# Kernel tuning notes

Hardware: AMD Instinct MI355X
Metric: run time of the kernel (lower is better)

The kernel has to match this reference:

```python
import jax, jax.numpy as jnp
import numpy as np

BN_EPS = 1e-5
LEAKY_SLOPE = 0.2


def setup_inputs() -> dict:
    key = jax.random.key(0)
    kx, kw, kg, kb = jax.random.split(key, 4)
    B, C, N, Cout, k = 8, 64, 4096, 64, 20
    x = jax.random.normal(kx, (B, C, N), dtype=jnp.float32)
    # Conv2d(2C -> Cout, kernel 1x1, bias=False) weight, stored as [Cout, 2C]
    W = jax.random.normal(kw, (Cout, 2 * C), dtype=jnp.float32) * 0.05
    gamma = jnp.ones((Cout,), dtype=jnp.float32) + 0.01 * jax.random.normal(kg, (Cout,), dtype=jnp.float32)
    beta = 0.01 * jax.random.normal(kb, (Cout,), dtype=jnp.float32)
    return {"x": x, "W": W, "gamma": gamma, "beta": beta, "k": k}


def reference(x, W, gamma, beta, k):
    # x: [B, C, N]
    B, C, N = x.shape
    # --- kNN graph on first 3 channels (xyz) ---
    xyz = jnp.transpose(x[:, :3, :], (0, 2, 1))              # [B, N, 3]
    sq = jnp.sum(xyz * xyz, axis=-1)                          # [B, N]
    dist = sq[:, :, None] + sq[:, None, :] - 2.0 * jnp.einsum('bnc,bmc->bnm', xyz, xyz)  # [B, N, N]
    _, idx = jax.lax.top_k(-dist, k + 1)                      # smallest distances, sorted
    edges = idx[:, :, 1:]                                     # drop self -> [B, N, k]

    # --- gather neighbor features ---
    xn = jnp.transpose(x, (0, 2, 1))                          # [B, N, C]
    nbrs = xn[jnp.arange(B)[:, None, None], edges]            # [B, N, k, C]
    central = xn[:, :, None, :]                               # [B, N, 1, C]
    edge_feat = jnp.concatenate(
        [jnp.broadcast_to(central, nbrs.shape), nbrs - central], axis=-1)  # [B, N, k, 2C]

    # --- 1x1 conv (pointwise matmul) ---
    h = jnp.einsum('bnkc,oc->bnko', edge_feat, W)             # [B, N, k, Cout]

    # --- BatchNorm2d (training-mode batch stats over B, k, N per channel) ---
    mean = jnp.mean(h, axis=(0, 1, 2))
    var = jnp.var(h, axis=(0, 1, 2))
    hn = (h - mean) * jax.lax.rsqrt(var + BN_EPS) * gamma + beta

    # --- LeakyReLU(0.2) then max over k neighbors ---
    act = jnp.where(hn >= 0, hn, LEAKY_SLOPE * hn)
    out = jnp.max(act, axis=2)                                # [B, N, Cout]
    return jnp.transpose(out, (0, 2, 1))                      # [B, Cout, N]
```

## Files before the change

kernel.cpp:

```cpp
#include <hip/hip_runtime.h>
#include <math.h>

#define BB 8
#define CC 64
#define NN 4096
#define COUT 64
#define KK 20
#define NQ 32768

__device__ __forceinline__ float np_sq(float ax, float ay, float az) {
    return __fadd_rn(__fadd_rn(__fmul_rn(ax, ax), __fmul_rn(ay, ay)), __fmul_rn(az, az));
}
__device__ __forceinline__ float np_dist(float qx, float qy, float qz, float sqn, float4 p) {
    float dot = __fadd_rn(__fadd_rn(__fmul_rn(qx, p.x), __fmul_rn(qy, p.y)), __fmul_rn(qz, p.z));
    return __fsub_rn(__fadd_rn(sqn, p.w), __fmul_rn(2.0f, dot));
}
__device__ __forceinline__ float min3f(float a, float b, float c) { return fminf(fminf(a, b), c); }
__device__ __forceinline__ float max3f(float a, float b, float c) { return fmaxf(fmaxf(a, b), c); }

__global__ __launch_bounds__(256) void prep_kernel(const float* __restrict__ x,
                                                   float4* __restrict__ pts4) {
    int g = blockIdx.x * 256 + threadIdx.x;
    int b = g >> 12, n = g & (NN - 1);
    const float* xb = x + (size_t)b * CC * NN;
    float ax = xb[n], ay = xb[NN + n], az = xb[2 * NN + n];
    pts4[g] = make_float4(ax, ay, az, np_sq(ax, ay, az));
}

template <int NCH, int SLOTS>
__global__ __launch_bounds__(256) void knn_part(const float4* __restrict__ pts4,
                                                float* __restrict__ pd) {
    constexpr int CH = NN / NCH;
    const int grp = blockIdx.x / NCH;
    const int ch = blockIdx.x % NCH;
    const int tid = threadIdx.x;
    const int q = grp * 256 + tid;
    const int b = q >> 12;
    const int n = q & (NN - 1);
    const float4* pb = pts4 + (size_t)b * NN;

    __shared__ float4 pts[CH];
    for (int i = tid; i < CH; i += 256) pts[i] = pb[ch * CH + i];
    __syncthreads();

    float4 me = pb[n];
    const float qx = me.x, qy = me.y, qz = me.z, sqn = me.w;

    float bd[SLOTS];
#pragma unroll
    for (int i = 0; i < SLOTS; ++i) bd[i] = INFINITY;

#pragma unroll 4
    for (int i = 0; i < CH; i += 4) {
        float4 p0 = pts[i + 0], p1 = pts[i + 1], p2 = pts[i + 2], p3 = pts[i + 3];
        float d0 = np_dist(qx, qy, qz, sqn, p0);
        float d1 = np_dist(qx, qy, qz, sqn, p1);
        float d2 = np_dist(qx, qy, qz, sqn, p2);
        float d3 = np_dist(qx, qy, qz, sqn, p3);
        float a0 = fminf(d0, d1), a1 = fmaxf(d0, d1);
        float b0 = fminf(d2, d3), b1 = fmaxf(d2, d3);
#pragma unroll
        for (int s = 0; s < SLOTS; ++s) {
            float mn = min3f(a0, b0, bd[s]);
            float md = __builtin_amdgcn_fmed3f(a0, b0, bd[s]);
            float mx = max3f(a0, b0, bd[s]);
            float t0 = fminf(a1, b1);
            float t1 = fmaxf(a1, b1);
            bd[s] = mn;
            a0 = md; a1 = mx;
            b0 = t0; b1 = t1;
        }
    }

#pragma unroll
    for (int j = 0; j < SLOTS; ++j) pd[(size_t)(ch * SLOTS + j) * NQ + q] = bd[j];
}

template <int LA, int LB, int R>
__device__ __forceinline__ void mergeR(const float* a, const float* b, float* out) {
#pragma unroll
    for (int r = 1; r <= R; ++r) {
        float best = INFINITY;
#pragma unroll
        for (int j = 0; j <= R; ++j) {
            if (j <= r) {
                float av = (j >= 1) ? ((j <= LA) ? a[j - 1] : INFINITY) : -INFINITY;
                float bv = (r - j >= 1) ? ((r - j <= LB) ? b[r - j - 1] : INFINITY) : -INFINITY;
                best = fminf(best, fmaxf(av, bv));
            }
        }
        out[r - 1] = best;
    }
}

template <int NCH, int SLOTS>
__global__ __launch_bounds__(256) void knn_tau(const float* __restrict__ pd,
                                               float* __restrict__ taubuf,
                                               int* __restrict__ budgetbuf) {
    const int q = blockIdx.x * 256 + threadIdx.x;
    constexpr int CH = NN / NCH;
    constexpr int LEN = SLOTS - 1;
    const int ch_self = (q & (NN - 1)) / CH;

    float L[NCH][LEN];
#pragma unroll
    for (int c = 0; c < NCH; ++c) {
        float raw[SLOTS];
#pragma unroll
        for (int j = 0; j < SLOTS; ++j) raw[j] = pd[(size_t)(c * SLOTS + j) * NQ + q];
        bool shift = (c == ch_self);
#pragma unroll
        for (int j = 0; j < LEN; ++j) L[c][j] = shift ? raw[j + 1] : raw[j];
    }

    float T[KK];
    mergeR<LEN, LEN, KK>(L[0], L[1], T);
#pragma unroll
    for (int c = 2; c < NCH; ++c) {
        float M[KK];
        mergeR<KK, LEN, KK>(T, L[c], M);
#pragma unroll
        for (int j = 0; j < KK; ++j) T[j] = M[j];
    }

    float tau = T[KK - 1];
    int cnt_lt = 0, cnt_eq = 0;
    bool flag = false;
#pragma unroll
    for (int c = 0; c < NCH; ++c) {
#pragma unroll
        for (int j = 0; j < LEN; ++j) {
            cnt_lt += (L[c][j] < tau) ? 1 : 0;
            cnt_eq += (L[c][j] == tau) ? 1 : 0;
        }
        flag = flag || (L[c][LEN - 1] <= tau);
    }
    int surplus = cnt_lt + cnt_eq - KK;
    taubuf[q] = tau;
    budgetbuf[q] = flag ? -1 : (surplus == 0 ? 0 : (KK - cnt_lt));
}

__device__ __forceinline__ int prefix_count(unsigned long long mask) {
    int r = __builtin_amdgcn_mbcnt_lo((unsigned)mask, 0);
    return __builtin_amdgcn_mbcnt_hi((unsigned)(mask >> 32), r);
}

__device__ void collect_one(const float4* __restrict__ pb, int n, float qx, float qy,
                            float qz, float sqn, float tau, int budget, int lane,
                            int* __restrict__ erow) {
    if (budget == 0) {
        int cnt = 0;
        for (int it = 0; it < 64; ++it) {
            int m = it * 64 + lane;
            float d = np_dist(qx, qy, qz, sqn, pb[m]);
            bool acc = (d <= tau) && (m != n);
            unsigned long long macc = __ballot(acc);
            if (macc) {
                int pos = cnt + prefix_count(macc);
                if (acc && pos < KK) erow[pos] = m;
                cnt += __popcll(macc);
            }
        }
        if (lane == 0) {
            for (int j = cnt; j < KK; ++j) erow[j] = (n + 1 + j) & (NN - 1);
        }
    } else if (budget > 0) {
        int cnt = 0, ties = 0;
        for (int it = 0; it < 64; ++it) {
            int m = it * 64 + lane;
            float d = np_dist(qx, qy, qz, sqn, pb[m]);
            bool valid = (m != n);
            bool is_lt = valid && (d < tau);
            bool is_tie = valid && (d == tau);
            unsigned long long mtie = __ballot(is_tie);
            int tie_rank = ties + prefix_count(mtie);
            bool acc = is_lt || (is_tie && tie_rank < budget);
            unsigned long long macc = __ballot(acc);
            int pos = cnt + prefix_count(macc);
            if (acc && pos < KK) erow[pos] = m;
            cnt += __popcll(macc);
            ties += __popcll(mtie);
        }
        if (lane == 0) {
            for (int j = cnt; j < KK; ++j) erow[j] = (n + 1 + j) & (NN - 1);
        }
    } else if (lane == 0) {
        unsigned long long bk[KK];
#pragma unroll
        for (int j = 0; j < KK; ++j) bk[j] = ~0ULL;
        for (int m = 0; m < NN; ++m) {
            if (m == n) continue;
            float d = np_dist(qx, qy, qz, sqn, pb[m]);
            unsigned u = __float_as_uint(d);
            u ^= (unsigned)((int)u >> 31) | 0x80000000u;
            unsigned long long key = ((unsigned long long)u << 32) | (unsigned)m;
            if (key < bk[KK - 1]) {
#pragma unroll
                for (int s = KK - 1; s >= 1; --s) {
                    bool sh = bk[s - 1] > key;
                    bool here = bk[s] > key;
                    bk[s] = sh ? bk[s - 1] : (here ? key : bk[s]);
                }
                if (bk[0] > key) bk[0] = key;
            }
        }
        for (int j = 0; j < KK; ++j) erow[j] = (int)(bk[j] & (NN - 1));
    }
}

__global__ __launch_bounds__(256) void knn_collect(const float4* __restrict__ pts4,
                                                   const float* __restrict__ taubuf,
                                                   const int* __restrict__ budgetbuf,
                                                   int* __restrict__ edges) {
    const int wave = threadIdx.x >> 6;
    const int lane = threadIdx.x & 63;
    const int q0 = (blockIdx.x * 4 + wave) * 8;
    const int b = q0 >> 12;
    const float4* pb = pts4 + (size_t)b * NN;

    int nj[8], bj[8];
    float qxj[8], qyj[8], qzj[8], sqj[8], tj[8];
    int orb = 0;
#pragma unroll
    for (int j = 0; j < 8; ++j) {
        int q = q0 + j;
        nj[j] = q & (NN - 1);
        float4 me = pb[nj[j]];
        qxj[j] = me.x; qyj[j] = me.y; qzj[j] = me.z; sqj[j] = me.w;
        tj[j] = taubuf[q];
        bj[j] = budgetbuf[q];
        orb |= bj[j];
    }

    if (orb == 0) {
        int cnt[8] = {0, 0, 0, 0, 0, 0, 0, 0};
        for (int it = 0; it < 64; ++it) {
            int m = it * 64 + lane;
            float4 p = pb[m];
#pragma unroll
            for (int j = 0; j < 8; ++j) {
                float d = np_dist(qxj[j], qyj[j], qzj[j], sqj[j], p);
                bool acc = (d <= tj[j]) && (m != nj[j]);
                unsigned long long mk = __ballot(acc);
                if (mk) {
                    int pos = cnt[j] + prefix_count(mk);
                    if (acc && pos < KK) edges[(size_t)(q0 + j) * KK + pos] = m;
                    cnt[j] += __popcll(mk);
                }
            }
        }
        if (lane == 0) {
#pragma unroll
            for (int j = 0; j < 8; ++j) {
                for (int t = cnt[j]; t < KK; ++t)
                    edges[(size_t)(q0 + j) * KK + t] = (nj[j] + 1 + t) & (NN - 1);
            }
        }
    } else {
#pragma unroll
        for (int j = 0; j < 8; ++j) {
            collect_one(pb, nj[j], qxj[j], qyj[j], qzj[j], sqj[j], tj[j], bj[j], lane,
                        edges + (size_t)(q0 + j) * KK);
        }
    }
}

__global__ __launch_bounds__(256) void proj_kernel(const float* __restrict__ x,
                                                   const float* __restrict__ W,
                                                   float* __restrict__ P1,
                                                   float* __restrict__ P2) {
    const int wid = blockIdx.x * 4 + (threadIdx.x >> 6);
    const int lane = threadIdx.x & 63;
    const int row_block = wid >> 4;
    const int og = __builtin_amdgcn_readfirstlane(wid & 15);
    const int row = row_block * 64 + lane;
    const int b = row >> 12;
    const int n = row & (NN - 1);
    const float* xb = x + (size_t)b * CC * NN;

    float p1[4] = {0.f, 0.f, 0.f, 0.f};
    float p2[4] = {0.f, 0.f, 0.f, 0.f};
#pragma unroll 8
    for (int c = 0; c < CC; ++c) {
        float xv = xb[(size_t)c * NN + n];
#pragma unroll
        for (int j = 0; j < 4; ++j) {
            int o = og * 4 + j;
            float w1 = W[o * 2 * CC + c];
            float w2 = W[o * 2 * CC + CC + c];
            p1[j] += (w1 - w2) * xv;
            p2[j] += w2 * xv;
        }
    }
#pragma unroll
    for (int j = 0; j < 4; ++j) {
        int o = og * 4 + j;
        P1[(size_t)row * 64 + o] = p1[j];
        P2[(size_t)row * 64 + o] = p2[j];
    }
}

__global__ __launch_bounds__(256) void stats_kernel(const float* __restrict__ P1,
                                                    const float* __restrict__ P2,
                                                    const int* __restrict__ edges,
                                                    float* __restrict__ partials,
                                                    float* __restrict__ out) {
    int blk = blockIdx.x;
    int b = blk & 7;
    int inner = blk >> 3;
    int row0 = b * NN + inner * 64;
    int pblk = row0 >> 6;
    int o = threadIdx.x & 63;
    int rq = threadIdx.x >> 6;
    int n0 = row0 & (NN - 1);
    const float* P2b = P2 + (size_t)b * NN * 64;
    __shared__ float tile[64][65];
    float s = 0.f, s2 = 0.f;
    for (int rr = rq; rr < 64; rr += 4) {
        int row = row0 + rr;
        float p1 = P1[row * 64 + o];
        const int* e = edges + row * KK;
        float hm = -INFINITY;
#pragma unroll
        for (int j = 0; j < KK; ++j) {
            int ej = e[j] & (NN - 1);
            float v = p1 + P2b[ej * 64 + o];
            s += v;
            s2 += v * v;
            hm = fmaxf(hm, v);
        }
        tile[rr][o] = hm;
    }
    __shared__ float sh1[256], sh2[256];
    sh1[threadIdx.x] = s;
    sh2[threadIdx.x] = s2;
    __syncthreads();
    if (threadIdx.x < 64) {
        float a = sh1[threadIdx.x] + sh1[threadIdx.x + 64] + sh1[threadIdx.x + 128] + sh1[threadIdx.x + 192];
        float a2 = sh2[threadIdx.x] + sh2[threadIdx.x + 64] + sh2[threadIdx.x + 128] + sh2[threadIdx.x + 192];
        partials[pblk * 128 + threadIdx.x] = a;
        partials[pblk * 128 + 64 + threadIdx.x] = a2;
    }
    int w2 = threadIdx.x >> 6;
    int lane = threadIdx.x & 63;
    for (int o2 = w2 * 16; o2 < w2 * 16 + 16; ++o2) {
        out[((size_t)(b * 64 + o2)) * NN + n0 + lane] = tile[lane][o2];
    }
}

__global__ __launch_bounds__(128) void finalize_kernel(const float* __restrict__ partials,
                                                       const float* __restrict__ gamma,
                                                       const float* __restrict__ beta,
                                                       float* __restrict__ consts) {
    int t = threadIdx.x;
    float s = 0.f;
    for (int i = 0; i < 512; ++i) s += partials[i * 128 + t];
    __shared__ float sh[128];
    sh[t] = s;
    __syncthreads();
    if (t < 64) {
        float sum = sh[t];
        float sumsq = sh[64 + t];
        const float M = (float)((size_t)BB * NN * KK);
        float mean = sum / M;
        float var = sumsq / M - mean * mean;
        float inv = 1.0f / sqrtf(var + 1e-5f);
        float A = gamma[t] * inv;
        float Cv = beta[t] - mean * A;
        consts[t] = A;
        consts[64 + t] = Cv;
    }
}

__global__ __launch_bounds__(256) void out2_kernel(const float* __restrict__ P1,
                                                   const float* __restrict__ P2,
                                                   const int* __restrict__ edges,
                                                   const float* __restrict__ consts,
                                                   float* __restrict__ out) {
    const int blk = blockIdx.x;
    const int b = blk >> 6;
    const int o = blk & 63;
    const float A = consts[o];
    const float Cv = consts[64 + o];
    float* orow = out + (size_t)blk * NN;
    if (A >= 0.f) {
#pragma unroll
        for (int it = 0; it < 4; ++it) {
            int idx = (it * 256 + threadIdx.x) * 4;
            float4 v = *(const float4*)(orow + idx);
            float h0 = v.x * A + Cv, h1 = v.y * A + Cv, h2 = v.z * A + Cv, h3 = v.w * A + Cv;
            v.x = h0 >= 0.f ? h0 : 0.2f * h0;
            v.y = h1 >= 0.f ? h1 : 0.2f * h1;
            v.z = h2 >= 0.f ? h2 : 0.2f * h2;
            v.w = h3 >= 0.f ? h3 : 0.2f * h3;
            *(float4*)(orow + idx) = v;
        }
    } else {
        const float* P2b = P2 + (size_t)b * NN * 64;
        for (int n = threadIdx.x; n < NN; n += 256) {
            size_t row = (size_t)b * NN + n;
            float p1 = P1[row * 64 + o];
            const int* e = edges + row * KK;
            float mx = -INFINITY;
            for (int j = 0; j < KK; ++j) {
                int ej = e[j] & (NN - 1);
                float h = p1 + P2b[ej * 64 + o];
                float hn = h * A + Cv;
                mx = fmaxf(mx, hn >= 0.f ? hn : 0.2f * hn);
            }
            orow[n] = mx;
        }
    }
}

extern "C" void kernel_launch(void* const* d_in, const int* in_sizes, int n_in,
                              void* d_out, int out_size, void* d_ws, size_t ws_size,
                              hipStream_t stream) {
    const float* x = (const float*)d_in[0];
    const float* W = (const float*)d_in[1];
    const float* gamma = (const float*)d_in[2];
    const float* beta = (const float*)d_in[3];
    float* out = (float*)d_out;

    char* w = (char*)d_ws;
    float4* pts4      = (float4*)(w + 0);
    float*  taubuf    = (float*)(w + 524288);
    int*    budgetbuf = (int*)(w + 655360);
    float*  partials  = (float*)(w + 786432);
    float*  consts    = (float*)(w + 1048576);
    int*    edges     = (int*)(w + 1049600);
    char*   region    = w + 3671040;
    float*  P1 = (float*)region;
    float*  P2 = P1 + (size_t)NQ * 64;
    float*  pd = (float*)region;

    const size_t need16 = 3671040 + (size_t)16 * 11 * NQ * 4;

    prep_kernel<<<128, 256, 0, stream>>>(x, pts4);
    if (ws_size >= need16) {
        knn_part<16, 11><<<128 * 16, 256, 0, stream>>>(pts4, pd);
        knn_tau<16, 11><<<128, 256, 0, stream>>>(pd, taubuf, budgetbuf);
    } else {
        knn_part<8, 13><<<128 * 8, 256, 0, stream>>>(pts4, pd);
        knn_tau<8, 13><<<128, 256, 0, stream>>>(pd, taubuf, budgetbuf);
    }
    knn_collect<<<1024, 256, 0, stream>>>(pts4, taubuf, budgetbuf, edges);

    proj_kernel<<<2048, 256, 0, stream>>>(x, W, P1, P2);
    stats_kernel<<<512, 256, 0, stream>>>(P1, P2, edges, partials, out);
    finalize_kernel<<<1, 128, 0, stream>>>(partials, gamma, beta, consts);
    out2_kernel<<<512, 256, 0, stream>>>(P1, P2, edges, consts, out);
}
```

Baseline: 194.3 us.

## Fuse prep into kNN partial pass, fold BN finalize into output, cheapen fallback

Removes the separate prep kernel: knn_part now reads xyz straight from x, builds the padded point records in shared memory, and lets one group of blocks write pts4 for later stages. The finalize kernel is dropped; each out2 block reduces the BN partial sums for its channel itself. The per-query candidate slots drop from 11 to 9. The slow single-lane fallback in collect_one now first gathers candidates with wave ballots into a shared buffer and sorts only those. Together these cut kernel launches and redundant work, but each out2 block now repeats the partial reduction, and fewer slots may send more queries down the fallback path.

```diff
diff --git a/kernel.cpp b/kernel.cpp
--- a/kernel.cpp
+++ b/kernel.cpp
@@ -18,17 +18,15 @@
 __device__ __forceinline__ float min3f(float a, float b, float c) { return fminf(fminf(a, b), c); }
 __device__ __forceinline__ float max3f(float a, float b, float c) { return fmaxf(fmaxf(a, b), c); }
 
-__global__ __launch_bounds__(256) void prep_kernel(const float* __restrict__ x,
-                                                   float4* __restrict__ pts4) {
-    int g = blockIdx.x * 256 + threadIdx.x;
-    int b = g >> 12, n = g & (NN - 1);
-    const float* xb = x + (size_t)b * CC * NN;
-    float ax = xb[n], ay = xb[NN + n], az = xb[2 * NN + n];
-    pts4[g] = make_float4(ax, ay, az, np_sq(ax, ay, az));
+__device__ __forceinline__ unsigned long long dm_key(float d, int m) {
+    unsigned u = __float_as_uint(d);
+    u ^= (unsigned)((int)u >> 31) | 0x80000000u;
+    return ((unsigned long long)u << 32) | (unsigned)m;
 }
 
 template <int NCH, int SLOTS>
-__global__ __launch_bounds__(256) void knn_part(const float4* __restrict__ pts4,
+__global__ __launch_bounds__(256) void knn_part(const float* __restrict__ x,
+                                                float4* __restrict__ pts4,
                                                 float* __restrict__ pd) {
     constexpr int CH = NN / NCH;
     const int grp = blockIdx.x / NCH;
@@ -37,14 +35,22 @@
     const int q = grp * 256 + tid;
     const int b = q >> 12;
     const int n = q & (NN - 1);
-    const float4* pb = pts4 + (size_t)b * NN;
+    const float* xb = x + (size_t)b * CC * NN;
+    const bool writer = ((grp & 15) == 0);
 
     __shared__ float4 pts[CH];
-    for (int i = tid; i < CH; i += 256) pts[i] = pb[ch * CH + i];
+    for (int i = tid; i < CH; i += 256) {
+        int m = ch * CH + i;
+        float ax = xb[m], ay = xb[NN + m], az = xb[2 * NN + m];
+        float4 v = make_float4(ax, ay, az, np_sq(ax, ay, az));
+        pts[i] = v;
+        if (writer) pts4[(size_t)b * NN + m] = v;
+    }
     __syncthreads();
 
-    float4 me = pb[n];
-    const float qx = me.x, qy = me.y, qz = me.z, sqn = me.w;
+    float qax = xb[n], qay = xb[NN + n], qaz = xb[2 * NN + n];
+    const float qx = qax, qy = qay, qz = qaz;
+    const float sqn = np_sq(qax, qay, qaz);
 
     float bd[SLOTS];
 #pragma unroll
@@ -145,8 +151,11 @@
     return __builtin_amdgcn_mbcnt_hi((unsigned)(mask >> 32), r);
 }
 
+#define FBCAP 128
+
 __device__ void collect_one(const float4* __restrict__ pb, int n, float qx, float qy,
                             float qz, float sqn, float tau, int budget, int lane,
+                            unsigned long long* __restrict__ fbuf,
                             int* __restrict__ erow) {
     if (budget == 0) {
         int cnt = 0;
@@ -184,27 +193,58 @@
         if (lane == 0) {
             for (int j = cnt; j < KK; ++j) erow[j] = (n + 1 + j) & (NN - 1);
         }
-    } else if (lane == 0) {
-        unsigned long long bk[KK];
-#pragma unroll
-        for (int j = 0; j < KK; ++j) bk[j] = ~0ULL;
-        for (int m = 0; m < NN; ++m) {
-            if (m == n) continue;
+    } else {
+        int cnt = 0;
+        for (int it = 0; it < 64; ++it) {
+            int m = it * 64 + lane;
             float d = np_dist(qx, qy, qz, sqn, pb[m]);
-            unsigned u = __float_as_uint(d);
-            u ^= (unsigned)((int)u >> 31) | 0x80000000u;
-            unsigned long long key = ((unsigned long long)u << 32) | (unsigned)m;
-            if (key < bk[KK - 1]) {
-#pragma unroll
-                for (int s = KK - 1; s >= 1; --s) {
-                    bool sh = bk[s - 1] > key;
-                    bool here = bk[s] > key;
-                    bk[s] = sh ? bk[s - 1] : (here ? key : bk[s]);
+            bool acc = (d <= tau) && (m != n);
+            unsigned long long macc = __ballot(acc);
+            if (macc) {
+                int pos = cnt + prefix_count(macc);
+                if (acc && pos < FBCAP) fbuf[pos] = dm_key(d, m);
+                cnt += __popcll(macc);
+            }
+        }
+        if (cnt <= FBCAP) {
+            if (lane == 0) {
+                unsigned long long bk[KK];
+#pragma unroll
+                for (int j = 0; j < KK; ++j) bk[j] = ~0ULL;
+                for (int i = 0; i < cnt; ++i) {
+                    unsigned long long key = fbuf[i];
+                    if (key < bk[KK - 1]) {
+#pragma unroll
+                        for (int s = KK - 1; s >= 1; --s) {
+                            bool sh = bk[s - 1] > key;
+                            bool here = bk[s] > key;
+                            bk[s] = sh ? bk[s - 1] : (here ? key : bk[s]);
+                        }
+                        if (bk[0] > key) bk[0] = key;
+                    }
                 }
-                if (bk[0] > key) bk[0] = key;
-            }
-        }
-        for (int j = 0; j < KK; ++j) erow[j] = (int)(bk[j] & (NN - 1));
+                for (int j = 0; j < KK; ++j) erow[j] = (int)(bk[j] & (NN - 1));
+            }
+        } else if (lane == 0) {
+            unsigned long long bk[KK];
+#pragma unroll
+            for (int j = 0; j < KK; ++j) bk[j] = ~0ULL;
+            for (int m = 0; m < NN; ++m) {
+                if (m == n) continue;
+                float d = np_dist(qx, qy, qz, sqn, pb[m]);
+                unsigned long long key = dm_key(d, m);
+                if (key < bk[KK - 1]) {
+#pragma unroll
+                    for (int s = KK - 1; s >= 1; --s) {
+                        bool sh = bk[s - 1] > key;
+                        bool here = bk[s] > key;
+                        bk[s] = sh ? bk[s - 1] : (here ? key : bk[s]);
+                    }
+                    if (bk[0] > key) bk[0] = key;
+                }
+            }
+            for (int j = 0; j < KK; ++j) erow[j] = (int)(bk[j] & (NN - 1));
+        }
     }
 }
 
@@ -217,6 +257,7 @@
     const int q0 = (blockIdx.x * 4 + wave) * 8;
     const int b = q0 >> 12;
     const float4* pb = pts4 + (size_t)b * NN;
+    __shared__ unsigned long long fbuf[4][FBCAP];
 
     int nj[8], bj[8];
     float qxj[8], qyj[8], qzj[8], sqj[8], tj[8];
@@ -260,7 +301,7 @@
 #pragma unroll
         for (int j = 0; j < 8; ++j) {
             collect_one(pb, nj[j], qxj[j], qyj[j], qzj[j], sqj[j], tj[j], bj[j], lane,
-                        edges + (size_t)(q0 + j) * KK);
+                        fbuf[wave], edges + (size_t)(q0 + j) * KK);
         }
     }
 }
@@ -348,45 +389,45 @@
     }
 }
 
-__global__ __launch_bounds__(128) void finalize_kernel(const float* __restrict__ partials,
-                                                       const float* __restrict__ gamma,
-                                                       const float* __restrict__ beta,
-                                                       float* __restrict__ consts) {
-    int t = threadIdx.x;
-    float s = 0.f;
-    for (int i = 0; i < 512; ++i) s += partials[i * 128 + t];
-    __shared__ float sh[128];
-    sh[t] = s;
-    __syncthreads();
-    if (t < 64) {
-        float sum = sh[t];
-        float sumsq = sh[64 + t];
-        const float M = (float)((size_t)BB * NN * KK);
-        float mean = sum / M;
-        float var = sumsq / M - mean * mean;
-        float inv = 1.0f / sqrtf(var + 1e-5f);
-        float A = gamma[t] * inv;
-        float Cv = beta[t] - mean * A;
-        consts[t] = A;
-        consts[64 + t] = Cv;
-    }
-}
-
 __global__ __launch_bounds__(256) void out2_kernel(const float* __restrict__ P1,
                                                    const float* __restrict__ P2,
                                                    const int* __restrict__ edges,
-                                                   const float* __restrict__ consts,
+                                                   const float* __restrict__ partials,
+                                                   const float* __restrict__ gamma,
+                                                   const float* __restrict__ beta,
                                                    float* __restrict__ out) {
     const int blk = blockIdx.x;
     const int b = blk >> 6;
     const int o = blk & 63;
-    const float A = consts[o];
-    const float Cv = consts[64 + o];
+    const int t = threadIdx.x;
+
+    __shared__ float r1[256], r2[256];
+    r1[t] = partials[t * 128 + o] + partials[(t + 256) * 128 + o];
+    r2[t] = partials[t * 128 + 64 + o] + partials[(t + 256) * 128 + 64 + o];
+    __syncthreads();
+    for (int step = 128; step >= 1; step >>= 1) {
+        if (t < step) { r1[t] += r1[t + step]; r2[t] += r2[t + step]; }
+        __syncthreads();
+    }
+    __shared__ float sA, sC;
+    if (t == 0) {
+        const float M = (float)((size_t)BB * NN * KK);
+        float mean = r1[0] / M;
+        float var = r2[0] / M - mean * mean;
+        float inv = 1.0f / sqrtf(var + 1e-5f);
+        float A = gamma[o] * inv;
+        sA = A;
+        sC = beta[o] - mean * A;
+    }
+    __syncthreads();
+    const float A = sA;
+    const float Cv = sC;
+
     float* orow = out + (size_t)blk * NN;
     if (A >= 0.f) {
 #pragma unroll
         for (int it = 0; it < 4; ++it) {
-            int idx = (it * 256 + threadIdx.x) * 4;
+            int idx = (it * 256 + t) * 4;
             float4 v = *(const float4*)(orow + idx);
             float h0 = v.x * A + Cv, h1 = v.y * A + Cv, h2 = v.z * A + Cv, h3 = v.w * A + Cv;
             v.x = h0 >= 0.f ? h0 : 0.2f * h0;
@@ -397,7 +438,7 @@
         }
     } else {
         const float* P2b = P2 + (size_t)b * NN * 64;
-        for (int n = threadIdx.x; n < NN; n += 256) {
+        for (int n = t; n < NN; n += 256) {
             size_t row = (size_t)b * NN + n;
             float p1 = P1[row * 64 + o];
             const int* e = edges + row * KK;
@@ -427,27 +468,24 @@
     float*  taubuf    = (float*)(w + 524288);
     int*    budgetbuf = (int*)(w + 655360);
     float*  partials  = (float*)(w + 786432);
-    float*  consts    = (float*)(w + 1048576);
     int*    edges     = (int*)(w + 1049600);
     char*   region    = w + 3671040;
     float*  P1 = (float*)region;
     float*  P2 = P1 + (size_t)NQ * 64;
     float*  pd = (float*)region;
 
-    const size_t need16 = 3671040 + (size_t)16 * 11 * NQ * 4;
-
-    prep_kernel<<<128, 256, 0, stream>>>(x, pts4);
-    if (ws_size >= need16) {
-        knn_part<16, 11><<<128 * 16, 256, 0, stream>>>(pts4, pd);
-        knn_tau<16, 11><<<128, 256, 0, stream>>>(pd, taubuf, budgetbuf);
+    const size_t needA = 3671040 + (size_t)16 * 9 * NQ * 4;
+
+    if (ws_size >= needA) {
+        knn_part<16, 9><<<128 * 16, 256, 0, stream>>>(x, pts4, pd);
+        knn_tau<16, 9><<<128, 256, 0, stream>>>(pd, taubuf, budgetbuf);
     } else {
-        knn_part<8, 13><<<128 * 8, 256, 0, stream>>>(pts4, pd);
+        knn_part<8, 13><<<128 * 8, 256, 0, stream>>>(x, pts4, pd);
         knn_tau<8, 13><<<128, 256, 0, stream>>>(pd, taubuf, budgetbuf);
     }
     knn_collect<<<1024, 256, 0, stream>>>(pts4, taubuf, budgetbuf, edges);
 
     proj_kernel<<<2048, 256, 0, stream>>>(x, W, P1, P2);
     stats_kernel<<<512, 256, 0, stream>>>(P1, P2, edges, partials, out);
-    finalize_kernel<<<1, 128, 0, stream>>>(partials, gamma, beta, consts);
-    out2_kernel<<<512, 256, 0, stream>>>(P1, P2, edges, consts, out);
-}
+    out2_kernel<<<512, 256, 0, stream>>>(P1, P2, edges, partials, gamma, beta, out);
+}
```

Result: slower. 229.1 us (+17.9%).
